# Kernel optimization log

Measured on AMD Instinct MI355X. Metric: run time of the kernel, lower is better.

## Reference

```python
import jax, jax.numpy as jnp
import numpy as np

B, S, D, H, DK, F = 4, 2048, 1024, 16, 64, 4096


def layer_norm(x, g, b, eps=1e-5):
    mu = jnp.mean(x, axis=-1, keepdims=True)
    var = jnp.var(x, axis=-1, keepdims=True)
    return (x - mu) * jax.lax.rsqrt(var + eps) * g + b


def setup_inputs() -> dict:
    key = jax.random.key(0)
    ks = jax.random.split(key, 16)
    s = 0.02
    return {
        "src": jax.random.normal(ks[0], (B, S, D), jnp.float32),
        # per-head q/k/v projections stacked over heads: (H, D, DK)
        "Wq": jax.random.normal(ks[1], (H, D, DK), jnp.float32) * s,
        "bq": jnp.zeros((H, DK), jnp.float32),
        "Wk": jax.random.normal(ks[2], (H, D, DK), jnp.float32) * s,
        "bk": jnp.zeros((H, DK), jnp.float32),
        "Wv": jax.random.normal(ks[3], (H, D, DK), jnp.float32) * s,
        "bv": jnp.zeros((H, DK), jnp.float32),
        "Wo": jax.random.normal(ks[4], (H * DK, D), jnp.float32) * s,
        "bo": jnp.zeros((D,), jnp.float32),
        "ln1_g": jnp.ones((D,), jnp.float32),
        "ln1_b": jnp.zeros((D,), jnp.float32),
        "W1": jax.random.normal(ks[5], (D, F), jnp.float32) * s,
        "b1": jnp.zeros((F,), jnp.float32),
        "W2": jax.random.normal(ks[6], (F, D), jnp.float32) * s,
        "b2": jnp.zeros((D,), jnp.float32),
        "ln2_g": jnp.ones((D,), jnp.float32),
        "ln2_b": jnp.zeros((D,), jnp.float32),
    }


def reference(src, Wq, bq, Wk, bk, Wv, bv, Wo, bo, ln1_g, ln1_b, W1, b1, W2, b2, ln2_g, ln2_b):
    # --- multi-head attention (all heads batched via einsum) ---
    q = jnp.einsum("bsd,hdk->bhsk", src, Wq) + bq[None, :, None, :]
    k = jnp.einsum("bsd,hdk->bhsk", src, Wk) + bk[None, :, None, :]
    v = jnp.einsum("bsd,hdk->bhsk", src, Wv) + bv[None, :, None, :]
    scale = jnp.sqrt(jnp.asarray(DK, q.dtype))
    scores = jnp.einsum("bhqk,bhsk->bhqs", q, k) / scale  # [B,H,S,S]
    p = jax.nn.softmax(scores, axis=-1)
    ctx = jnp.einsum("bhqs,bhsk->bhqk", p, v)             # [B,H,S,DK]
    ctx = ctx.transpose(0, 2, 1, 3).reshape(src.shape[0], src.shape[1], H * DK)
    attn_out = ctx @ Wo + bo
    x = layer_norm(src + attn_out, ln1_g, ln1_b)
    # --- feed-forward ---
    ff = jax.nn.relu(x @ W1 + b1) @ W2 + b2
    return layer_norm(x + ff, ln2_g, ln2_b)
```

## Files before the change

kernel.cpp:

```cpp
#include <hip/hip_runtime.h>
#include <hip/hip_bf16.h>
#include <cstddef>
#include <cstdint>

typedef __bf16 bf16;
typedef __bf16 bf16x4 __attribute__((ext_vector_type(4)));
typedef __bf16 bf16x8 __attribute__((ext_vector_type(8)));
typedef float f32x4 __attribute__((ext_vector_type(4)));
typedef float f32x16 __attribute__((ext_vector_type(16)));
typedef unsigned int u32x4 __attribute__((ext_vector_type(4)));

#define GLD_LDS16(g, l) __builtin_amdgcn_global_load_lds( \
    (const __attribute__((address_space(1))) void*)(g),   \
    (__attribute__((address_space(3))) void*)(l), 16, 0, 0)

#define SBAR __builtin_amdgcn_s_barrier()
#define SCHED0 __builtin_amdgcn_sched_barrier(0)
#define VMW(n) asm volatile("s_waitcnt vmcnt(" #n ")" ::: "memory")

static __device__ inline unsigned int cvtpk(float lo, float hi) {
  unsigned int r;
  asm("v_cvt_pk_bf16_f32 %0, %1, %2" : "=v"(r) : "v"(lo), "v"(hi));
  return r;
}
static __device__ inline void plswap(unsigned int& a, unsigned int& b) {
  asm("v_permlane32_swap_b32 %0, %1" : "+v"(a), "+v"(b));
}
static __device__ inline float fexp2(float x) {
#if __has_builtin(__builtin_amdgcn_exp2f)
  return __builtin_amdgcn_exp2f(x);
#else
  float r; asm("v_exp_f32 %0, %1" : "=v"(r) : "v"(x)); return r;
#endif
}
static __device__ inline float tsum16(const float* e) {
  float s0 = e[0] + e[1], s1 = e[2] + e[3], s2 = e[4] + e[5], s3 = e[6] + e[7];
  float s4 = e[8] + e[9], s5 = e[10] + e[11], s6 = e[12] + e[13], s7 = e[14] + e[15];
  return ((s0 + s1) + (s2 + s3)) + ((s4 + s5) + (s6 + s7));
}

__global__ void __launch_bounds__(256)
k_cast(const float* __restrict__ in, bf16* __restrict__ out) {
  int gid = blockIdx.x * 256 + threadIdx.x;
  f32x4 a = ((const f32x4*)in)[gid * 2];
  f32x4 b = ((const f32x4*)in)[gid * 2 + 1];
  bf16x8 o;
#pragma unroll
  for (int i = 0; i < 4; ++i) { o[i] = (bf16)a[i]; o[i + 4] = (bf16)b[i]; }
  ((bf16x8*)out)[gid] = o;
}

__global__ void __launch_bounds__(256)
k_transpose_t(const float* __restrict__ in, bf16* __restrict__ out, int R, int C) {
  __shared__ float tile[64][68];
  const int nct = C >> 6;
  const int bc = blockIdx.x % nct, br = blockIdx.x / nct;
  const int r0 = br << 6, c0 = bc << 6;
  const int t = threadIdx.x;
  const int tr = t >> 4, tc4 = (t & 15) << 2;
#pragma unroll
  for (int i = 0; i < 4; ++i)
    *(f32x4*)&tile[i * 16 + tr][tc4] =
        *(const f32x4*)&in[(size_t)(r0 + i * 16 + tr) * C + c0 + tc4];
  __syncthreads();
  const int c = t >> 2, rch = (t & 3) << 4;
  bf16 ob[16];
#pragma unroll
  for (int j = 0; j < 16; ++j) ob[j] = (bf16)tile[rch + j][c];
  bf16* dst = out + (size_t)(c0 + c) * R + r0 + rch;
  *(bf16x8*)&dst[0] = *(bf16x8*)&ob[0];
  *(bf16x8*)&dst[8] = *(bf16x8*)&ob[8];
}

__global__ void __launch_bounds__(256)
k_reorder_qkv_t(const float* __restrict__ Wq, const float* __restrict__ Wk,
                const float* __restrict__ Wv, bf16* __restrict__ WqkvT) {
  __shared__ float tile[64][68];
  const int bid = blockIdx.x;
  const int sub = bid >> 4, tl = bid & 15;
  const int proj = sub >> 4, h = sub & 15;
  const float* W = (proj == 0) ? Wq : (proj == 1) ? Wk : Wv;
  const float* src = W + (size_t)h * 65536;
  const int r0 = tl << 6;
  const int t = threadIdx.x, tr = t >> 4, tc4 = (t & 15) << 2;
#pragma unroll
  for (int i = 0; i < 4; ++i)
    *(f32x4*)&tile[i * 16 + tr][tc4] =
        *(const f32x4*)&src[(size_t)(r0 + i * 16 + tr) * 64 + tc4];
  __syncthreads();
  const int c = t >> 2, rch = (t & 3) << 4;
  bf16 ob[16];
#pragma unroll
  for (int j = 0; j < 16; ++j) ob[j] = (bf16)tile[rch + j][c];
  bf16* dst = WqkvT + ((size_t)(proj * 1024 + h * 64 + c)) * 1024 + r0 + rch;
  *(bf16x8*)&dst[0] = *(bf16x8*)&ob[0];
  *(bf16x8*)&dst[8] = *(bf16x8*)&ob[8];
}

__global__ void __launch_bounds__(256)
k_bias_qkv(const float* __restrict__ bq, const float* __restrict__ bk,
           const float* __restrict__ bv, float* __restrict__ bqkv) {
  int n = blockIdx.x * 256 + threadIdx.x;
  int proj = n >> 10, wi = n & 1023;
  const float* bb = (proj == 0) ? bq : (proj == 1) ? bk : bv;
  bqkv[n] = bb[wi];
}

template <int MODE, int NREP>
__global__ void __launch_bounds__(512, 1)
k_gemm4(const bf16* __restrict__ A, const bf16* __restrict__ Bt,
        const float* __restrict__ bias, void* __restrict__ outp,
        int M, int N, int K, int klen, int splitk,
        bf16* __restrict__ qb, bf16* __restrict__ kb, bf16* __restrict__ vb) {
  constexpr int BN = 128 * NREP;
  constexpr int BROWS = 64 * NREP;
  __shared__ __align__(16) bf16 Asl[4][8192];
  __shared__ __align__(16) bf16 Bsl[4][BROWS * 64];

  const int tid = threadIdx.x;
  const int lane = tid & 63, wave = tid >> 6;
  const int l16 = lane & 15, lq = lane >> 4;
  const int qwm = wave >> 2, qwn = wave & 3;

  const int tiles = gridDim.x / splitk;
  const int twg = blockIdx.x % tiles;
  const int sk = blockIdx.x / tiles;
  const int k0 = sk * klen;
  const int mtiles = M >> 8;
  const int tile_m = (twg % mtiles) << 8;
  const int tile_n = (twg / mtiles) * BN;

  const bf16* Abase = A + (size_t)tile_m * K + k0;
  const bf16* Bbase = Bt + (size_t)tile_n * K + k0;

  const int crow = tid >> 3;
  const int ccol = ((tid & 7) ^ (crow & 7)) << 3;

  auto stageA = [&](int T, int h, int slot) {
    const bf16* s_ = Abase + (size_t)(h * 128 + crow) * K + T * 64 + ccol;
    GLD_LDS16(s_, &Asl[slot][tid * 8]);
    GLD_LDS16(s_ + (size_t)64 * K, &Asl[slot][tid * 8 + 4096]);
  };
  auto stageB = [&](int T, int h, int slot) {
    const bf16* s_ = Bbase + (size_t)(h * BROWS + crow) * K + T * 64 + ccol;
    GLD_LDS16(s_, &Bsl[slot][tid * 8]);
    if (NREP == 2) GLD_LDS16(s_ + (size_t)64 * K, &Bsl[slot][tid * 8 + 4096]);
  };

  const int xk = l16 & 7;
  const int swz0 = (lq ^ xk) * 16;
  const int swz1 = ((4 | lq) ^ xk) * 16;
  const int arow_b = (qwm * 64 + l16) * 128;
  const int brow_b = (qwn * 16 * NREP + l16) * 128;

  bf16x8 af[4][2];
  bf16x8 bb[2][NREP][2];
  f32x4 acc[2][2][4][NREP] = {};

  auto dsA = [&](int slot) {
    const char* Ab = (const char*)&Asl[slot][0] + arow_b;
#pragma unroll
    for (int mi = 0; mi < 4; ++mi) {
      af[mi][0] = *(const bf16x8*)(Ab + mi * 2048 + swz0);
      af[mi][1] = *(const bf16x8*)(Ab + mi * 2048 + swz1);
    }
  };
  auto dsB2 = [&](int slot0, int slot1) {
    const char* B0 = (const char*)&Bsl[slot0][0] + brow_b;
    const char* B1 = (const char*)&Bsl[slot1][0] + brow_b;
#pragma unroll
    for (int ni = 0; ni < NREP; ++ni) {
      bb[0][ni][0] = *(const bf16x8*)(B0 + ni * 2048 + swz0);
      bb[0][ni][1] = *(const bf16x8*)(B0 + ni * 2048 + swz1);
      bb[1][ni][0] = *(const bf16x8*)(B1 + ni * 2048 + swz0);
      bb[1][ni][1] = *(const bf16x8*)(B1 + ni * 2048 + swz1);
    }
  };
  auto MF2 = [&](int mh) {
    __builtin_amdgcn_s_setprio(1);
#pragma unroll
    for (int nh = 0; nh < 2; ++nh)
#pragma unroll
      for (int mi = 0; mi < 4; ++mi)
#pragma unroll
        for (int ni = 0; ni < NREP; ++ni)
#pragma unroll
          for (int p = 0; p < 2; ++p)
            acc[mh][nh][mi][ni] = __builtin_amdgcn_mfma_f32_16x16x32_bf16(
                af[mi][p], bb[nh][ni][p], acc[mh][nh][mi][ni], 0, 0, 0);
    __builtin_amdgcn_s_setprio(0);
  };

  const int NT = klen >> 6;
  const int NI = NT >> 1;

  stageA(0, 0, 0); stageA(0, 1, 1); stageB(0, 0, 0); stageB(0, 1, 1);
  stageA(1, 0, 2); stageB(1, 0, 2); stageB(1, 1, 3);
  SCHED0;
  if (NREP == 2) { VMW(6); } else { VMW(4); }
  SBAR;

  for (int i = 0; i < NI; ++i) {
    const int t2 = 2 * i + 2, t3 = 2 * i + 3;
    const bool tv = (t2 < NT);
    dsA(0); dsB2(0, 1);
    stageA(2 * i + 1, 1, 3);
    SBAR; MF2(0); SBAR;
    dsA(1);
    if (tv) { stageA(t2, 0, 0); stageB(t2, 0, 0); }
    SCHED0;
    if (!tv) { VMW(0); }
    else if (NREP == 2) { VMW(4); } else { VMW(3); }
    SBAR; MF2(1); SBAR;
    dsA(2); dsB2(2, 3);
    if (tv) { stageA(t2, 1, 1); stageB(t2, 1, 1); }
    SBAR; MF2(0); SBAR;
    dsA(3);
    if (tv) {
      stageA(t3, 0, 2); stageB(t3, 0, 2); stageB(t3, 1, 3);
      SCHED0;
      if (NREP == 2) { VMW(6); } else { VMW(4); }
    }
    SBAR; MF2(1); SBAR;
  }

  float* psplit = (MODE == 3) ? ((float*)outp + (size_t)sk * M * N) : nullptr;
#pragma unroll
  for (int mh = 0; mh < 2; ++mh)
#pragma unroll
    for (int nh = 0; nh < 2; ++nh)
#pragma unroll
      for (int mi = 0; mi < 4; ++mi)
#pragma unroll
        for (int ni = 0; ni < NREP; ++ni) {
          const int gn = tile_n + nh * (BN / 2) + qwn * 16 * NREP + ni * 16 + l16;
          const float bv = (MODE == 3) ? 0.f : bias[gn];
          f32x4 v = acc[mh][nh][mi][ni];
          const int gm0 = tile_m + mh * 128 + qwm * 64 + mi * 16 + lq * 4;
          if (MODE == 0) {
            int proj = gn >> 10, wi = gn & 1023;
            int h = wi >> 6, dk = wi & 63;
            int b = gm0 >> 11, sdx = gm0 & 2047;
            size_t bhs = (size_t)((b << 4) + h);
            if (proj == 0) {
#pragma unroll
              for (int i2 = 0; i2 < 4; ++i2)
                qb[(bhs * 2048 + sdx + i2) * 64 + dk] = (bf16)((v[i2] + bv) * 0.18033688f);
            } else if (proj == 1) {
#pragma unroll
              for (int i2 = 0; i2 < 4; ++i2)
                kb[(bhs * 2048 + sdx + i2) * 64 + dk] = (bf16)(v[i2] + bv);
            } else {
              bf16x4 pk;
#pragma unroll
              for (int i2 = 0; i2 < 4; ++i2) pk[i2] = (bf16)(v[i2] + bv);
              *(bf16x4*)&vb[(bhs * 64 + dk) * 2048 + sdx] = pk;
            }
          } else if (MODE == 1) {
#pragma unroll
            for (int i2 = 0; i2 < 4; ++i2)
              ((bf16*)outp)[(size_t)(gm0 + i2) * N + gn] = (bf16)(v[i2] + bv);
          } else if (MODE == 2) {
#pragma unroll
            for (int i2 = 0; i2 < 4; ++i2)
              ((bf16*)outp)[(size_t)(gm0 + i2) * N + gn] = (bf16)fmaxf(v[i2] + bv, 0.f);
          } else {
#pragma unroll
            for (int i2 = 0; i2 < 4; ++i2)
              psplit[(size_t)(gm0 + i2) * N + gn] = v[i2];
          }
        }
}

__global__ void __launch_bounds__(256, 2)
k_attn(const bf16* __restrict__ qb, const bf16* __restrict__ kb,
       const bf16* __restrict__ vb, bf16* __restrict__ ctx) {
  __shared__ __align__(16) bf16 KsL[3][4096];
  __shared__ __align__(16) bf16 VsL[3][4096];

  const int bid = blockIdx.x;
  const int wg = (bid & 7) * 64 + (bid >> 3);
  const int bh = wg >> 3, qt = wg & 7;

  const bf16* Qp  = qb + (size_t)bh * 131072 + (size_t)qt * 16384;
  const bf16* Kbh = kb + (size_t)bh * 131072;
  const bf16* Vbh = vb + (size_t)bh * 131072;

  const int tid = threadIdx.x, wave = tid >> 6, lane = tid & 63;
  const int l31 = lane & 31, hi = lane >> 5;

  bf16x8 qfA[4], qfB[4];
  {
    const bf16* qra = Qp + (size_t)(wave * 64 + l31) * 64 + hi * 8;
    const bf16* qrb = qra + 32 * 64;
#pragma unroll
    for (int kd = 0; kd < 4; ++kd) {
      qfA[kd] = *(const bf16x8*)(qra + kd * 16);
      qfB[kd] = *(const bf16x8*)(qrb + kd * 16);
    }
  }

  const int c0 = tid, c1 = tid + 256;
  const int sw0 = ((c0 ^ (c0 >> 3)) & 7) * 8, rw0 = c0 >> 3;
  const int sw1 = ((c1 ^ (c1 >> 3)) & 7) * 8, rw1 = c1 >> 3;
  const int kof0 = rw0 * 64 + sw0, kof1 = rw1 * 64 + sw1;
  const int vof0 = rw0 * 2048 + sw0, vof1 = rw1 * 2048 + sw1;

  const int xr = (hi << 4) ^ ((l31 & 7) << 4);
  const int rb = l31 * 128 + xr;

  f32x16 oA[2] = {}, oB[2] = {};
  float lA = 0.f, lB = 0.f;

#define STAGE_KV(buf, s0)                                             \
  do {                                                                \
    GLD_LDS16(Kbh + (size_t)(s0) * 64 + kof0, &KsL[buf][c0 * 8]);     \
    GLD_LDS16(Kbh + (size_t)(s0) * 64 + kof1, &KsL[buf][c1 * 8]);     \
    GLD_LDS16(Vbh + (s0) + vof0, &VsL[buf][c0 * 8]);                  \
    GLD_LDS16(Vbh + (s0) + vof1, &VsL[buf][c1 * 8]);                  \
  } while (0)

  STAGE_KV(0, 0);
  STAGE_KV(1, 64);

  int cur = 0;
  for (int kt = 0; kt < 32; ++kt) {
    SCHED0;
    if (kt == 31) { VMW(0); }
    else          { VMW(4); }
    __builtin_amdgcn_s_barrier();
    SCHED0;

    if (kt < 30) {
      int nx = cur + 2; if (nx >= 3) nx -= 3;
      STAGE_KV(nx, (kt + 2) * 64);
    }

    const char* Kc = (const char*)&KsL[cur][0];
    const char* Vc = (const char*)&VsL[cur][0];

    bf16x8 paA[4], paB[4];
#pragma unroll
    for (int st = 0; st < 2; ++st) {
      f32x16 sA = {}, sB = {};
      __builtin_amdgcn_s_setprio(1);
#pragma unroll
      for (int kd = 0; kd < 4; ++kd) {
        bf16x8 a = *(const bf16x8*)(Kc + st * 4096 + (rb ^ (kd << 5)));
        sA = __builtin_amdgcn_mfma_f32_32x32x16_bf16(a, qfA[kd], sA, 0, 0, 0);
        sB = __builtin_amdgcn_mfma_f32_32x32x16_bf16(a, qfB[kd], sB, 0, 0, 0);
      }
      __builtin_amdgcn_s_setprio(0);

      float eA[16], eB[16];
#pragma unroll
      for (int i = 0; i < 16; ++i) {
        eA[i] = fexp2(sA[i]);
        eB[i] = fexp2(sB[i]);
      }
      lA += tsum16(eA);
      lB += tsum16(eB);
      unsigned int qdA[4][2], qdB[4][2];
#pragma unroll
      for (int g = 0; g < 4; ++g)
#pragma unroll
        for (int w = 0; w < 2; ++w) {
          qdA[g][w] = cvtpk(eA[g * 4 + w * 2], eA[g * 4 + w * 2 + 1]);
          qdB[g][w] = cvtpk(eB[g * 4 + w * 2], eB[g * 4 + w * 2 + 1]);
        }
#pragma unroll
      for (int a2 = 0; a2 < 2; ++a2) {
        unsigned int x0 = qdA[2 * a2][0], y0 = qdA[2 * a2 + 1][0];
        unsigned int x1 = qdA[2 * a2][1], y1 = qdA[2 * a2 + 1][1];
        plswap(x0, y0); plswap(x1, y1);
        u32x4 fA = {x0, x1, y0, y1};
        paA[st * 2 + a2] = __builtin_bit_cast(bf16x8, fA);
        unsigned int u0 = qdB[2 * a2][0], v0 = qdB[2 * a2 + 1][0];
        unsigned int u1 = qdB[2 * a2][1], v1 = qdB[2 * a2 + 1][1];
        plswap(u0, v0); plswap(u1, v1);
        u32x4 fB = {u0, u1, v0, v1};
        paB[st * 2 + a2] = __builtin_bit_cast(bf16x8, fB);
      }
    }

    __builtin_amdgcn_s_setprio(1);
#pragma unroll
    for (int nd = 0; nd < 2; ++nd)
#pragma unroll
      for (int ks = 0; ks < 4; ++ks) {
        bf16x8 vf = *(const bf16x8*)(Vc + nd * 4096 + (rb ^ (ks << 5)));
        oA[nd] = __builtin_amdgcn_mfma_f32_32x32x16_bf16(paA[ks], vf, oA[nd], 0, 0, 0);
        oB[nd] = __builtin_amdgcn_mfma_f32_32x32x16_bf16(paB[ks], vf, oB[nd], 0, 0, 0);
      }
    __builtin_amdgcn_s_setprio(0);

    if (++cur == 3) cur = 0;
  }
#undef STAGE_KV

  const float ltA = lA + __shfl_xor(lA, 32);
  const float ltB = lB + __shfl_xor(lB, 32);
  const float ivA = 1.f / ltA;
  const float ivB = 1.f / ltB;

  const int b = bh >> 4, h = bh & 15;
  const size_t rowbase = (size_t)(b * 2048 + qt * 256 + wave * 64);
#pragma unroll
  for (int r = 0; r < 16; ++r) {
    const int qr = (r & 3) + 8 * (r >> 2) + 4 * hi;
    const float dA = __shfl(ivA, qr);
    const float dB = __shfl(ivB, qr);
#pragma unroll
    for (int nd = 0; nd < 2; ++nd) {
      const int dk = nd * 32 + l31;
      ctx[(rowbase + qr) * 1024 + h * 64 + dk]      = (bf16)(oA[nd][r] * dA);
      ctx[(rowbase + 32 + qr) * 1024 + h * 64 + dk] = (bf16)(oB[nd][r] * dB);
    }
  }
}

template <typename RT, typename DT, typename OT>
__global__ void __launch_bounds__(256)
k_ln(const RT* __restrict__ resid, const DT* __restrict__ delta,
     const float* __restrict__ g, const float* __restrict__ bta,
     OT* __restrict__ out) {
  const int row = blockIdx.x, tid = threadIdx.x;
  const int wave = tid >> 6, lane = tid & 63;
  __shared__ float rs_[4], rs2_[4];
  const RT* r = resid + (size_t)row * 1024;
  const DT* d = delta + (size_t)row * 1024;
  OT* o = out + (size_t)row * 1024;
  float x[4], s = 0.f, s2 = 0.f;
#pragma unroll
  for (int j = 0; j < 4; ++j) {
    int idx = tid + j * 256;
    float v = (float)r[idx] + (float)d[idx];
    x[j] = v; s += v; s2 += v * v;
  }
#pragma unroll
  for (int m = 32; m >= 1; m >>= 1) { s += __shfl_xor(s, m); s2 += __shfl_xor(s2, m); }
  if (lane == 0) { rs_[wave] = s; rs2_[wave] = s2; }
  __syncthreads();
  float ts = rs_[0] + rs_[1] + rs_[2] + rs_[3];
  float ts2 = rs2_[0] + rs2_[1] + rs2_[2] + rs2_[3];
  float mean = ts * (1.f / 1024.f);
  float var = ts2 * (1.f / 1024.f) - mean * mean;
  float rstd = rsqrtf(var + 1e-5f);
#pragma unroll
  for (int j = 0; j < 4; ++j) {
    int idx = tid + j * 256;
    o[idx] = (OT)((x[j] - mean) * rstd * g[idx] + bta[idx]);
  }
}

__global__ void __launch_bounds__(256)
k_ln_sk(const bf16* __restrict__ x1r, const float* __restrict__ p0,
        const float* __restrict__ p1, const float* __restrict__ bias,
        const float* __restrict__ g, const float* __restrict__ bta,
        float* __restrict__ out) {
  const int row = blockIdx.x, tid = threadIdx.x;
  const int wave = tid >> 6, lane = tid & 63;
  __shared__ float rs_[4], rs2_[4];
  const bf16* r = x1r + (size_t)row * 1024;
  const float* a = p0 + (size_t)row * 1024;
  const float* b = p1 + (size_t)row * 1024;
  float* o = out + (size_t)row * 1024;
  float x[4], s = 0.f, s2 = 0.f;
#pragma unroll
  for (int j = 0; j < 4; ++j) {
    int idx = tid + j * 256;
    float v = (float)r[idx] + a[idx] + b[idx] + bias[idx];
    x[j] = v; s += v; s2 += v * v;
  }
#pragma unroll
  for (int m = 32; m >= 1; m >>= 1) { s += __shfl_xor(s, m); s2 += __shfl_xor(s2, m); }
  if (lane == 0) { rs_[wave] = s; rs2_[wave] = s2; }
  __syncthreads();
  float ts = rs_[0] + rs_[1] + rs_[2] + rs_[3];
  float ts2 = rs2_[0] + rs2_[1] + rs2_[2] + rs2_[3];
  float mean = ts * (1.f / 1024.f);
  float var = ts2 * (1.f / 1024.f) - mean * mean;
  float rstd = rsqrtf(var + 1e-5f);
#pragma unroll
  for (int j = 0; j < 4; ++j) {
    int idx = tid + j * 256;
    o[idx] = (x[j] - mean) * rstd * g[idx] + bta[idx];
  }
}

extern "C" void kernel_launch(void* const* d_in, const int* in_sizes, int n_in,
                              void* d_out, int out_size, void* d_ws, size_t ws_size,
                              hipStream_t stream) {
  const float* src  = (const float*)d_in[0];
  const float* Wq   = (const float*)d_in[1];
  const float* bq   = (const float*)d_in[2];
  const float* Wk   = (const float*)d_in[3];
  const float* bk   = (const float*)d_in[4];
  const float* Wv   = (const float*)d_in[5];
  const float* bv   = (const float*)d_in[6];
  const float* Wo   = (const float*)d_in[7];
  const float* bo   = (const float*)d_in[8];
  const float* ln1g = (const float*)d_in[9];
  const float* ln1b = (const float*)d_in[10];
  const float* W1   = (const float*)d_in[11];
  const float* b1   = (const float*)d_in[12];
  const float* W2   = (const float*)d_in[13];
  const float* b2   = (const float*)d_in[14];
  const float* ln2g = (const float*)d_in[15];
  const float* ln2b = (const float*)d_in[16];

  char* p = (char*)d_ws;
  bf16*  WqkvT = (bf16*)p;  p += (size_t)3072 * 1024 * 2;
  float* bqkv  = (float*)p; p += 16384;
  bf16*  WoT   = (bf16*)p;  p += (size_t)1024 * 1024 * 2;
  bf16*  W1T   = (bf16*)p;  p += (size_t)4096 * 1024 * 2;
  bf16*  W2T   = (bf16*)p;  p += (size_t)1024 * 4096 * 2;
  bf16*  srcb  = (bf16*)p;  p += (size_t)8388608 * 2;
  bf16*  qbuf  = (bf16*)p;  p += (size_t)8388608 * 2;
  bf16*  kbuf  = (bf16*)p;  p += (size_t)8388608 * 2;
  bf16*  vbuf  = (bf16*)p;  p += (size_t)8388608 * 2;
  bf16*  ctx   = (bf16*)p;  p += (size_t)8388608 * 2;
  bf16*  x1    = (bf16*)p;  p += (size_t)8388608 * 2;
  bf16*  ff1   = (bf16*)p;  p += (size_t)8192 * 4096 * 2;
  bf16*  tmp   = qbuf;
  float* pk0   = (float*)srcb;

  k_cast<<<4096, 256, 0, stream>>>(src, srcb);
  k_reorder_qkv_t<<<768, 256, 0, stream>>>(Wq, Wk, Wv, WqkvT);
  k_bias_qkv<<<12, 256, 0, stream>>>(bq, bk, bv, bqkv);
  k_transpose_t<<<256, 256, 0, stream>>>(Wo, WoT, 1024, 1024);
  k_transpose_t<<<1024, 256, 0, stream>>>(W1, W1T, 1024, 4096);
  k_transpose_t<<<1024, 256, 0, stream>>>(W2, W2T, 4096, 1024);

  k_gemm4<0, 1><<<768, 512, 0, stream>>>(srcb, WqkvT, bqkv, nullptr,
                                         8192, 3072, 1024, 1024, 1, qbuf, kbuf, vbuf);
  k_attn<<<512, 256, 0, stream>>>(qbuf, kbuf, vbuf, ctx);
  k_gemm4<1, 1><<<256, 512, 0, stream>>>(ctx, WoT, bo, tmp,
                                         8192, 1024, 1024, 1024, 1, nullptr, nullptr, nullptr);
  k_ln<float, bf16, bf16><<<8192, 256, 0, stream>>>(src, tmp, ln1g, ln1b, x1);
  k_gemm4<2, 2><<<512, 512, 0, stream>>>(x1, W1T, b1, ff1,
                                         8192, 4096, 1024, 1024, 1, nullptr, nullptr, nullptr);
  k_gemm4<3, 2><<<256, 512, 0, stream>>>(ff1, W2T, nullptr, pk0,
                                         8192, 1024, 4096, 2048, 2, nullptr, nullptr, nullptr);
  k_ln_sk<<<8192, 256, 0, stream>>>(x1, pk0, pk0 + (size_t)8192 * 1024, b2,
                                    ln2g, ln2b, (float*)d_out);
}
```

Measured before the change: 482.2 us.

## Use split-K for output projection, larger QKV tiles, and finer-grained load waits

The GEMM main loop gains extra partial vmcnt waits before each MFMA phase. Loads are now waited on incrementally instead of all at once, so more of them can stay in flight. The QKV projection switches to the NREP=2 tile configuration with half the blocks. The output projection now uses a 2-way split-K into fp32 partials, with bias, residual and layernorm fused into a templated k_ln_sk. This trades extra fp32 partial traffic for more parallelism in the 256-block output GEMM.

```diff
diff --git a/kernel.cpp b/kernel.cpp
--- a/kernel.cpp
+++ b/kernel.cpp
@@ -205,15 +205,20 @@
     const bool tv = (t2 < NT);
     dsA(0); dsB2(0, 1);
     stageA(2 * i + 1, 1, 3);
+    SCHED0;
+    if (NREP == 2) { VMW(10); } else { VMW(7); }
     SBAR; MF2(0); SBAR;
     dsA(1);
     if (tv) { stageA(t2, 0, 0); stageB(t2, 0, 0); }
     SCHED0;
-    if (!tv) { VMW(0); }
-    else if (NREP == 2) { VMW(4); } else { VMW(3); }
+    if (!tv) { VMW(2); }
+    else if (NREP == 2) { VMW(6); } else { VMW(5); }
     SBAR; MF2(1); SBAR;
     dsA(2); dsB2(2, 3);
     if (tv) { stageA(t2, 1, 1); stageB(t2, 1, 1); }
+    SCHED0;
+    if (!tv) { VMW(0); }
+    else if (NREP == 2) { VMW(8); } else { VMW(6); }
     SBAR; MF2(0); SBAR;
     dsA(3);
     if (tv) {
@@ -419,22 +424,24 @@
   }
 }
 
-template <typename RT, typename DT, typename OT>
+template <typename RT, typename OT>
 __global__ void __launch_bounds__(256)
-k_ln(const RT* __restrict__ resid, const DT* __restrict__ delta,
-     const float* __restrict__ g, const float* __restrict__ bta,
-     OT* __restrict__ out) {
+k_ln_sk(const RT* __restrict__ resid, const float* __restrict__ p0,
+        const float* __restrict__ p1, const float* __restrict__ bias,
+        const float* __restrict__ g, const float* __restrict__ bta,
+        OT* __restrict__ out) {
   const int row = blockIdx.x, tid = threadIdx.x;
   const int wave = tid >> 6, lane = tid & 63;
   __shared__ float rs_[4], rs2_[4];
   const RT* r = resid + (size_t)row * 1024;
-  const DT* d = delta + (size_t)row * 1024;
+  const float* a = p0 + (size_t)row * 1024;
+  const float* b = p1 + (size_t)row * 1024;
   OT* o = out + (size_t)row * 1024;
   float x[4], s = 0.f, s2 = 0.f;
 #pragma unroll
   for (int j = 0; j < 4; ++j) {
     int idx = tid + j * 256;
-    float v = (float)r[idx] + (float)d[idx];
+    float v = (float)r[idx] + a[idx] + b[idx] + bias[idx];
     x[j] = v; s += v; s2 += v * v;
   }
 #pragma unroll
@@ -450,41 +457,6 @@
   for (int j = 0; j < 4; ++j) {
     int idx = tid + j * 256;
     o[idx] = (OT)((x[j] - mean) * rstd * g[idx] + bta[idx]);
-  }
-}
-
-__global__ void __launch_bounds__(256)
-k_ln_sk(const bf16* __restrict__ x1r, const float* __restrict__ p0,
-        const float* __restrict__ p1, const float* __restrict__ bias,
-        const float* __restrict__ g, const float* __restrict__ bta,
-        float* __restrict__ out) {
-  const int row = blockIdx.x, tid = threadIdx.x;
-  const int wave = tid >> 6, lane = tid & 63;
-  __shared__ float rs_[4], rs2_[4];
-  const bf16* r = x1r + (size_t)row * 1024;
-  const float* a = p0 + (size_t)row * 1024;
-  const float* b = p1 + (size_t)row * 1024;
-  float* o = out + (size_t)row * 1024;
-  float x[4], s = 0.f, s2 = 0.f;
-#pragma unroll
-  for (int j = 0; j < 4; ++j) {
-    int idx = tid + j * 256;
-    float v = (float)r[idx] + a[idx] + b[idx] + bias[idx];
-    x[j] = v; s += v; s2 += v * v;
-  }
-#pragma unroll
-  for (int m = 32; m >= 1; m >>= 1) { s += __shfl_xor(s, m); s2 += __shfl_xor(s2, m); }
-  if (lane == 0) { rs_[wave] = s; rs2_[wave] = s2; }
-  __syncthreads();
-  float ts = rs_[0] + rs_[1] + rs_[2] + rs_[3];
-  float ts2 = rs2_[0] + rs2_[1] + rs2_[2] + rs2_[3];
-  float mean = ts * (1.f / 1024.f);
-  float var = ts2 * (1.f / 1024.f) - mean * mean;
-  float rstd = rsqrtf(var + 1e-5f);
-#pragma unroll
-  for (int j = 0; j < 4; ++j) {
-    int idx = tid + j * 256;
-    o[idx] = (x[j] - mean) * rstd * g[idx] + bta[idx];
   }
 }
 
@@ -522,8 +494,8 @@
   bf16*  ctx   = (bf16*)p;  p += (size_t)8388608 * 2;
   bf16*  x1    = (bf16*)p;  p += (size_t)8388608 * 2;
   bf16*  ff1   = (bf16*)p;  p += (size_t)8192 * 4096 * 2;
-  bf16*  tmp   = qbuf;
   float* pk0   = (float*)srcb;
+  float* pk1   = pk0 + (size_t)8192 * 1024;
 
   k_cast<<<4096, 256, 0, stream>>>(src, srcb);
   k_reorder_qkv_t<<<768, 256, 0, stream>>>(Wq, Wk, Wv, WqkvT);
@@ -532,16 +504,17 @@
   k_transpose_t<<<1024, 256, 0, stream>>>(W1, W1T, 1024, 4096);
   k_transpose_t<<<1024, 256, 0, stream>>>(W2, W2T, 4096, 1024);
 
-  k_gemm4<0, 1><<<768, 512, 0, stream>>>(srcb, WqkvT, bqkv, nullptr,
+  k_gemm4<0, 2><<<384, 512, 0, stream>>>(srcb, WqkvT, bqkv, nullptr,
                                          8192, 3072, 1024, 1024, 1, qbuf, kbuf, vbuf);
   k_attn<<<512, 256, 0, stream>>>(qbuf, kbuf, vbuf, ctx);
-  k_gemm4<1, 1><<<256, 512, 0, stream>>>(ctx, WoT, bo, tmp,
-                                         8192, 1024, 1024, 1024, 1, nullptr, nullptr, nullptr);
-  k_ln<float, bf16, bf16><<<8192, 256, 0, stream>>>(src, tmp, ln1g, ln1b, x1);
+  k_gemm4<3, 2><<<256, 512, 0, stream>>>(ctx, WoT, nullptr, pk0,
+                                         8192, 1024, 1024, 512, 2, nullptr, nullptr, nullptr);
+  k_ln_sk<float, bf16><<<8192, 256, 0, stream>>>(src, pk0, pk1, bo,
+                                                 ln1g, ln1b, x1);
   k_gemm4<2, 2><<<512, 512, 0, stream>>>(x1, W1T, b1, ff1,
                                          8192, 4096, 1024, 1024, 1, nullptr, nullptr, nullptr);
   k_gemm4<3, 2><<<256, 512, 0, stream>>>(ff1, W2T, nullptr, pk0,
                                          8192, 1024, 4096, 2048, 2, nullptr, nullptr, nullptr);
-  k_ln_sk<<<8192, 256, 0, stream>>>(x1, pk0, pk0 + (size_t)8192 * 1024, b2,
-                                    ln2g, ln2b, (float*)d_out);
-}
+  k_ln_sk<bf16, float><<<8192, 256, 0, stream>>>(x1, pk0, pk1, b2,
+                                                 ln2g, ln2b, (float*)d_out);
+}
```

Result: slower. 505.7 us (+4.9%).
